# Kernel tuning notes

Hardware: AMD Instinct MI355X
Metric: run time of the kernel (lower is better)

## Reference

```python
import jax, jax.numpy as jnp
import numpy as np

H = 128          # controller hidden size
NCELL = 8        # memory cells
CS = 8           # cell size
R = 1            # read heads
L = 16           # stacked DNC layers
E = 15           # embedding size
NCLS = 30
NUMFRI = 5
NN_IN = H + R * CS                   # 136, controller input width (layers > 0)
XI = R * CS + 3 * CS + 5 * R + 3     # 40, interface vector size
CLIP = 20.0
EPS = 1e-6
B, T = 128, 64
NOT_EYE = 1.0 - np.eye(NCELL, dtype=np.float32)


def setup_inputs() -> dict:
    key = jax.random.key(0)
    ks = iter(jax.random.split(key, 40))
    n = lambda shape, s=0.05: jax.random.normal(next(ks), shape, dtype=jnp.float32) * s
    return {
        "x": jax.random.randint(next(ks), (B, T), 0, NCLS, dtype=jnp.int32),
        "f": n((B, H * NUMFRI), 1.0),
        "embed": n((NCLS + 3, E), 1.0),
        # LSTM controller: [layer, sublayer(2), 4H, in] with in padded to NN_IN
        "W_ih": n((L, 2, 4 * H, NN_IN)),
        "W_hh": n((L, 2, 4 * H, H)),
        "b_ih": n((L, 2, 4 * H)),
        "b_hh": n((L, 2, 4 * H)),
        "W_if": n((XI, H)),            # memory interface
        "b_if": n((XI,)),
        "W_out": n((H, NN_IN)),        # final DNC output linear
        "b_out": n((H,)),
        "W_fri": n((H, H * NUMFRI)),
        "b_fri": n((H,)),
        "W_c1": n((H, 2 * H)),
        "b_c1": n((H,)),
        "W_c2": n((NCLS, H)),
        "b_c2": n((NCLS,)),
    }


def lstm_cell(x, h, c, wih, whh, bih, bhh):
    g = x @ wih.T + h @ whh.T + bih + bhh
    i, f, gg, o = jnp.split(g, 4, axis=-1)  # torch gate order i,f,g,o
    c2 = jax.nn.sigmoid(f) * c + jax.nn.sigmoid(i) * jnp.tanh(gg)
    h2 = jax.nn.sigmoid(o) * jnp.tanh(c2)
    return h2, c2


def content_weight(mem, keys, strengths):
    # cosine similarity between keys [b,h,cs] and memory rows [b,m,cs]
    mn = mem / (jnp.linalg.norm(mem, axis=2, keepdims=True) + EPS)
    kn = keys / (jnp.linalg.norm(keys, axis=2, keepdims=True) + EPS)
    sim = jnp.einsum('bhc,bmc->bhm', kn, mn)
    return jax.nn.softmax(sim * strengths[:, :, None], axis=2)


def allocate(usage):
    u = EPS + (1.0 - EPS) * usage
    phi = jnp.argsort(u, axis=1)          # free list (ascending usage)
    su = jnp.take_along_axis(u, phi, axis=1)
    shifted = jnp.cumprod(jnp.concatenate([jnp.ones_like(su[:, :1]), su], axis=1), axis=1)[:, :-1]
    sa = (1.0 - su) * shifted
    phi_rev = jnp.argsort(phi, axis=1)    # inverse permutation
    return jnp.take_along_axis(sa, phi_rev, axis=1)[:, None, :]   # [b,1,m]


def memory_step(xi, mstate):
    mem, link, prec, rw, ww, usage = mstate
    b = xi.shape[0]
    rk = jnp.tanh(xi[:, :R * CS].reshape(b, R, CS))
    rs = jax.nn.softplus(xi[:, R * CS:R * CS + R])
    wk = jnp.tanh(xi[:, R * CS + R:R * CS + R + CS].reshape(b, 1, CS))
    ws = jax.nn.softplus(xi[:, R * CS + R + CS:R * CS + R + CS + 1])
    er = jax.nn.sigmoid(xi[:, R * CS + R + CS + 1:R * CS + R + 2 * CS + 1].reshape(b, 1, CS))
    wv = jnp.tanh(xi[:, R * CS + R + 2 * CS + 1:R * CS + R + 3 * CS + 1].reshape(b, 1, CS))
    fg = jax.nn.sigmoid(xi[:, R * CS + R + 3 * CS + 1:R * CS + 2 * R + 3 * CS + 1])
    ag = jax.nn.sigmoid(xi[:, R * CS + 2 * R + 3 * CS + 1:R * CS + 2 * R + 3 * CS + 2])
    wg = jax.nn.sigmoid(xi[:, R * CS + 2 * R + 3 * CS + 2:R * CS + 2 * R + 3 * CS + 3])
    modes = jax.nn.softmax(xi[:, R * CS + 2 * R + 3 * CS + 3:].reshape(b, R, 3), axis=-1)
    # --- write ---
    usage = usage + (1 - usage) * (1 - jnp.prod(1 - ww, axis=1))
    psi = jnp.prod(1 - fg[:, :, None] * rw, axis=1)
    usage = usage * psi
    wcw = content_weight(mem, wk, ws)                  # [b,1,m]
    alloc = allocate(usage)
    a3 = ag[:, :, None]; g3 = wg[:, :, None]
    ww = g3 * (a3 * alloc + (1 - a3) * wcw)            # [b,1,m]
    reset = jnp.prod(1 - ww[:, :, :, None] * er[:, :, None, :], axis=1)  # [b,m,cs]
    mem = mem * reset + jnp.einsum('bhm,bhc->bmc', ww, wv)
    ww_i = ww[:, :, :, None]; ww_j = ww[:, :, None, :]
    link = (1 - ww_i - ww_j) * link + ww_i * prec[:, :, None, :]
    link = link * NOT_EYE[None, None]
    prec = (1 - jnp.sum(ww, axis=2, keepdims=True)) * prec + ww
    # --- read ---
    cw = content_weight(mem, rk, rs)                   # [b,r,m]
    fwdw = jnp.einsum('bhij,brj->brhi', link, rw)      # forward weightings
    bwdw = jnp.einsum('bri,bhij->brhj', rw, link)      # backward weightings
    rw = (modes[:, :, 2:3] * cw
          + jnp.sum(modes[:, :, 1:2][:, :, :, None] * fwdw, axis=2)
          + jnp.sum(modes[:, :, 0:1][:, :, :, None] * bwdw, axis=2))
    read_vecs = jnp.einsum('brm,bmc->brc', rw, mem).reshape(b, R * CS)
    return read_vecs, (mem, link, prec, rw, ww, usage)


def _forward(x, f, embed, W_ih, W_hh, b_ih, b_hh, W_if, b_if, W_out, b_out,
             W_fri, b_fri, W_c1, b_c1, W_c2, b_c2):
    b = x.shape[0]
    emb = embed[x]                                     # [b,t,E]
    carry0 = (jnp.zeros((L, 2, b, H), jnp.float32), jnp.zeros((L, 2, b, H), jnp.float32),
              jnp.zeros((b, NCELL, CS), jnp.float32), jnp.zeros((b, 1, NCELL, NCELL), jnp.float32),
              jnp.zeros((b, 1, NCELL), jnp.float32), jnp.zeros((b, R, NCELL), jnp.float32),
              jnp.zeros((b, 1, NCELL), jnp.float32), jnp.zeros((b, NCELL), jnp.float32))

    def step(carry, x_t):
        h, c, mem, link, prec, rw, ww, usage = carry
        inp = x_t   # layer-0 sees [x_t, zero initial read] (reset_experience=True); zeros come from padding
        hs, cs = [], []
        for l in range(L):
            xin = jnp.pad(inp, ((0, 0), (0, NN_IN - inp.shape[1])))
            h0, c0 = lstm_cell(xin, h[l, 0], c[l, 0], W_ih[l, 0], W_hh[l, 0], b_ih[l, 0], b_hh[l, 0])
            xin1 = jnp.pad(h0, ((0, 0), (0, NN_IN - H)))
            h1, c1 = lstm_cell(xin1, h[l, 1], c[l, 1], W_ih[l, 1], W_hh[l, 1], b_ih[l, 1], b_hh[l, 1])
            hs.append(jnp.stack([h0, h1])); cs.append(jnp.stack([c0, c1]))
            out = jnp.clip(h1, -CLIP, CLIP)
            xi = out @ W_if.T + b_if
            read_vecs, (mem, link, prec, rw, ww, usage) = memory_step(xi, (mem, link, prec, rw, ww, usage))
            inp = jnp.concatenate([out, read_vecs], axis=1)   # [b, 136] -> next layer
        y = inp @ W_out.T + b_out
        return (jnp.stack(hs), jnp.stack(cs), mem, link, prec, rw, ww, usage), y

    _, ys = jax.lax.scan(step, carry0, emb.transpose(1, 0, 2))
    z = ys[-1]                                         # encoder output = last timestep [b,H]
    f_out = jax.nn.relu(f @ W_fri.T + b_fri)
    hcat = jnp.concatenate([z, f_out], axis=1)         # [b,2H]
    h1 = jax.nn.relu(hcat @ W_c1.T + b_c1)
    return h1 @ W_c2.T + b_c2                          # [b, n_class]


def reference(x, f, embed, W_ih, W_hh, b_ih, b_hh, W_if, b_if, W_out, b_out,
              W_fri, b_fri, W_c1, b_c1, W_c2, b_c2):
    return _forward(x, f, embed, W_ih, W_hh, b_ih, b_hh, W_if, b_if, W_out, b_out,
                    W_fri, b_fri, W_c1, b_c1, W_c2, b_c2)
```

## Files before the change

kernel.cpp:

```cpp
#include <hip/hip_runtime.h>
#include <stdint.h>

#define LNUM 16
#define H 128
#define TT 64
#define NCLSN 30
#define EPSF 1e-6f

typedef _Float16 half2v __attribute__((ext_vector_type(2)));

__device__ inline float fdot2(uint32_t a, uint32_t b, float c) {
  return __builtin_amdgcn_fdot2(__builtin_bit_cast(half2v, a),
                                __builtin_bit_cast(half2v, b), c, false);
}
__device__ inline float dot8(uint4 w, uint4 xv, float a) {
  a = fdot2(w.x, xv.x, a); a = fdot2(w.y, xv.y, a);
  a = fdot2(w.z, xv.z, a); a = fdot2(w.w, xv.w, a);
  return a;
}
__device__ __forceinline__ float rcpf(float x) { return __builtin_amdgcn_rcpf(x); }
__device__ inline float sigf(float x) { return rcpf(1.0f + __expf(-x)); }
__device__ __forceinline__ float tanh_fast(float x) {
  float xc = fminf(fmaxf(x, -15.f), 15.f);
  float e = __expf(2.f * xc);
  return (e - 1.f) * rcpf(e + 1.f);
}
__device__ __forceinline__ float softplus_fast(float x) {
  return fmaxf(x, 0.f) + __logf(1.f + __expf(-fabsf(x)));
}
__device__ inline uint32_t packh2(float a, float b) {
  half2v h; h.x = (_Float16)a; h.y = (_Float16)b;
  return __builtin_bit_cast(uint32_t, h);
}
__device__ inline uint16_t f16bits(float a) {
  _Float16 h = (_Float16)a;
  return __builtin_bit_cast(uint16_t, h);
}
__device__ __forceinline__ void gl_lds16(const uint4* g, uint4* l) {
  __builtin_amdgcn_global_load_lds(
      (const __attribute__((address_space(1))) void*)g,
      (__attribute__((address_space(3))) void*)l, 16, 0, 0);
}
__device__ __forceinline__ void bar_lgkm() {
  asm volatile("s_waitcnt lgkmcnt(0)\ns_barrier" ::: "memory");
}

__global__ void prepA(const float* __restrict__ W_ih, const float* __restrict__ W_hh,
                      uint4* __restrict__ WB) {
  int idx = blockIdx.x * 256 + threadIdx.x;
  int lc = idx / 16896;
  int r  = idx % 16896;
  int row, kq;
  if (r < 16384) {
    int q = r >> 11;
    int rem = r & 2047;
    int g = rem >> 9;
    int gt = rem & 511;
    int j = gt >> 2, s = gt & 3;
    kq = s + 4 * q;
    row = g * 128 + j;
  } else {
    int r2 = r - 16384;
    int g = r2 >> 7, j = r2 & 127;
    kq = 32; row = g * 128 + j;
  }
  bool zero = ((lc & 1) && kq == 16);
  uint32_t p[4];
#pragma unroll
  for (int i2 = 0; i2 < 4; i2++) {
    float w0 = 0.f, w1 = 0.f;
    if (!zero) {
      int k0 = 8 * kq + 2 * i2;
      w0 = (k0 < 136) ? W_ih[((size_t)lc * 512 + row) * 136 + k0]
                      : W_hh[((size_t)lc * 512 + row) * 128 + (k0 - 136)];
      w1 = (k0 + 1 < 136) ? W_ih[((size_t)lc * 512 + row) * 136 + k0 + 1]
                          : W_hh[((size_t)lc * 512 + row) * 128 + (k0 + 1 - 136)];
    }
    p[i2] = packh2(w0, w1);
  }
  uint4 v; v.x = p[0]; v.y = p[1]; v.z = p[2]; v.w = p[3];
  WB[idx] = v;
}

__global__ void prepB(const float* __restrict__ b_ih, const float* __restrict__ b_hh,
                      const float* __restrict__ W_if, const float* __restrict__ W_fri,
                      const float* __restrict__ W_c1, const float* __restrict__ W_c2,
                      float* __restrict__ bias_comb, uint32_t* __restrict__ Wif16,
                      float* __restrict__ WfriT, float* __restrict__ Wc1T,
                      float* __restrict__ Wc2T) {
  int idx = blockIdx.x * 256 + threadIdx.x;
  if (idx < 16384) { bias_comb[idx] = b_ih[idx] + b_hh[idx]; return; }
  idx -= 16384;
  if (idx < 2560)  {
    int j = idx / 64, k2 = idx % 64;
    Wif16[idx] = packh2(W_if[j * 128 + 2 * k2], W_if[j * 128 + 2 * k2 + 1]);
    return;
  }
  idx -= 2560;
  if (idx < 81920) { int k = idx / 128, j = idx % 128; WfriT[idx] = W_fri[j * 640 + k]; return; }
  idx -= 81920;
  if (idx < 32768) { int k = idx / 128, j = idx % 128; Wc1T[idx]  = W_c1[j * 256 + k]; return; }
  idx -= 32768;
  if (idx < 3840)  { int k = idx / 30,  j = idx % 30;  Wc2T[idx]  = W_c2[j * 128 + k]; return; }
}

__device__ __forceinline__ void memstep_par(
    int m, const float* __restrict__ xi,
    float (&mm)[8], float (&lkr)[8],
    float& u, float& p, float& r, float& w,
    float (&rv)[8]) {
  float rk[8], wk[8], er[8], wv[8];
#pragma unroll
  for (int c = 0; c < 8; c++) {
    rk[c] = tanh_fast(xi[c]);
    wk[c] = tanh_fast(xi[9 + c]);
    er[c] = sigf(xi[18 + c]);
    wv[c] = tanh_fast(xi[26 + c]);
  }
  float rs  = softplus_fast(xi[8]);
  float wsd = softplus_fast(xi[17]);
  float fg  = sigf(xi[34]), ag = sigf(xi[35]), wg = sigf(xi[36]);
  float l0 = xi[37], l1 = xi[38], l2 = xi[39];
  float lmx = fmaxf(l0, fmaxf(l1, l2));
  float eb = __expf(l0 - lmx), ef = __expf(l1 - lmx), ec = __expf(l2 - lmx);
  float minv = rcpf(eb + ef + ec);
  float mode_b = eb * minv, mode_f = ef * minv, mode_c = ec * minv;

  u = u + (1.f - u) * w;
  u *= (1.f - fg * r);

  float kn2 = 0.f, mn2 = 0.f, dp = 0.f;
#pragma unroll
  for (int c = 0; c < 8; c++) { kn2 += wk[c]*wk[c]; mn2 += mm[c]*mm[c]; dp += wk[c]*mm[c]; }
  float sim = dp * rcpf((sqrtf(kn2) + EPSF) * (sqrtf(mn2) + EPSF)) * wsd;
  float mx = sim;
  mx = fmaxf(mx, __shfl_xor(mx, 1));
  mx = fmaxf(mx, __shfl_xor(mx, 2));
  mx = fmaxf(mx, __shfl_xor(mx, 4));
  float e = __expf(sim - mx);
  float se = e;
  se += __shfl_xor(se, 1); se += __shfl_xor(se, 2); se += __shfl_xor(se, 4);
  float wcw = e * rcpf(se);

  float up = EPSF + (1.f - EPSF) * u;
  float prod = 1.f;
#pragma unroll
  for (int n = 0; n < 8; n++) {
    float un = __shfl(up, n);
    bool before = (un < up) || (un == up && n < m);
    prod *= ((n != m) && before) ? un : 1.f;
  }
  float alloc = (1.f - up) * prod;
  float wn = wg * (ag * alloc + (1.f - ag) * wcw);
  float sw = wn;
  sw += __shfl_xor(sw, 1); sw += __shfl_xor(sw, 2); sw += __shfl_xor(sw, 4);

#pragma unroll
  for (int c = 0; c < 8; c++)
    mm[c] = mm[c] * (1.f - wn * er[c]) + wn * wv[c];

  float wnv[8], pvv[8];
#pragma unroll
  for (int n = 0; n < 8; n++) { wnv[n] = __shfl(wn, n); pvv[n] = __shfl(p, n); }
#pragma unroll
  for (int jj = 0; jj < 8; jj++)
    lkr[jj] = (jj == m) ? 0.f : ((1.f - wn - wnv[jj]) * lkr[jj] + wn * pvv[jj]);
  p = (1.f - sw) * p + wn;

  float rn2 = 0.f; mn2 = 0.f; dp = 0.f;
#pragma unroll
  for (int c = 0; c < 8; c++) { rn2 += rk[c]*rk[c]; mn2 += mm[c]*mm[c]; dp += rk[c]*mm[c]; }
  float sim2 = dp * rcpf((sqrtf(rn2) + EPSF) * (sqrtf(mn2) + EPSF)) * rs;
  float mx2 = sim2;
  mx2 = fmaxf(mx2, __shfl_xor(mx2, 1));
  mx2 = fmaxf(mx2, __shfl_xor(mx2, 2));
  mx2 = fmaxf(mx2, __shfl_xor(mx2, 4));
  float e2 = __expf(sim2 - mx2);
  float se2 = e2;
  se2 += __shfl_xor(se2, 1); se2 += __shfl_xor(se2, 2); se2 += __shfl_xor(se2, 4);
  float cw = e2 * rcpf(se2);

  float rv8[8];
#pragma unroll
  for (int n = 0; n < 8; n++) rv8[n] = __shfl(r, n);
  float fwd = 0.f;
#pragma unroll
  for (int jj = 0; jj < 8; jj++) fwd += lkr[jj] * rv8[jj];
  float bw[8];
#pragma unroll
  for (int jj = 0; jj < 8; jj++) bw[jj] = r * lkr[jj];
#pragma unroll
  for (int jj = 0; jj < 8; jj++) {
    bw[jj] += __shfl_xor(bw[jj], 1);
    bw[jj] += __shfl_xor(bw[jj], 2);
    bw[jj] += __shfl_xor(bw[jj], 4);
  }
  bool s1 = (m & 1) != 0, s2 = (m & 2) != 0, s4 = (m & 4) != 0;
  float t0 = s1 ? bw[1] : bw[0];
  float t1 = s1 ? bw[3] : bw[2];
  float t2 = s1 ? bw[5] : bw[4];
  float t3 = s1 ? bw[7] : bw[6];
  float q0 = s2 ? t1 : t0;
  float q1 = s2 ? t3 : t2;
  float bwd = s4 ? q1 : q0;

  float rn = mode_c * cw + mode_f * fwd + mode_b * bwd;

#pragma unroll
  for (int c = 0; c < 8; c++) rv[c] = rn * mm[c];
#pragma unroll
  for (int c = 0; c < 8; c++) {
    rv[c] += __shfl_xor(rv[c], 1);
    rv[c] += __shfl_xor(rv[c], 2);
    rv[c] += __shfl_xor(rv[c], 4);
  }
  r = rn; w = wn;
}

__device__ __forceinline__ void aux_work(
    int lane, bool write_inp,
    const uint4 (&wreg)[16], const float* __restrict__ b_if,
    const uint4* __restrict__ outhu4, float* __restrict__ xi_lds,
    uint4* __restrict__ inpu4,
    float (&mm)[8], float (&lkr)[8],
    float& u, float& p, float& r, float& w,
    float (&rv)[8]) {
  if (lane < 40) {
    float acc0 = 0.f;
#pragma unroll
    for (int q = 0; q < 16; q++) acc0 = dot8(wreg[q], outhu4[q], acc0);
    xi_lds[lane] = acc0 + b_if[lane];
  }
  asm volatile("s_waitcnt lgkmcnt(0)" ::: "memory");
  __builtin_amdgcn_sched_barrier(0);
  __builtin_amdgcn_wave_barrier();
  if (lane < 8) {
    memstep_par(lane, xi_lds, mm, lkr, u, p, r, w, rv);
    if (write_inp && lane == 0) {
      uint4 pv4;
      pv4.x = packh2(rv[0], rv[1]); pv4.y = packh2(rv[2], rv[3]);
      pv4.z = packh2(rv[4], rv[5]); pv4.w = packh2(rv[6], rv[7]);
      inpu4[16] = pv4;
    }
  }
}

#define STAGE(lcX, qX, bbX)                                                    \
  do {                                                                         \
    const uint4* sp_ = WB + (size_t)(lcX) * 16896 + (size_t)(qX) * 2048 + tid; \
    uint4* dp_ = myslab + (size_t)(bbX) * 256;                                 \
    gl_lds16(sp_,        dp_);                                                 \
    gl_lds16(sp_ + 512,  dp_ + 64);                                            \
    gl_lds16(sp_ + 1024, dp_ + 128);                                           \
    gl_lds16(sp_ + 1536, dp_ + 192);                                           \
  } while (0)

__global__ __launch_bounds__(576) void dnc_main(
    const int* __restrict__ x, const float* __restrict__ embed,
    const uint4* __restrict__ WB, const float* __restrict__ bias_comb,
    const uint32_t* __restrict__ Wif16, const float* __restrict__ b_if,
    const float* __restrict__ W_out, const float* __restrict__ b_out,
    float* __restrict__ y_buf) {
  __shared__ __align__(16) uint16_t hst[32 * 128];
  __shared__ float c_st[32 * 128];
  __shared__ float emb_lds[495];
  __shared__ __align__(16) uint32_t inp16[17 * 4];
  __shared__ __align__(16) uint16_t outh16[128];
  __shared__ float inp_f32[128];
  __shared__ float xi_lds[40];
  __shared__ float rv_f32[8];
  __shared__ __align__(16) uint4 sbuf[8 * 4 * 256];

  uint4* inpu4 = (uint4*)inp16;
  uint4* hstu4 = (uint4*)hst;
  uint4* outhu4 = (uint4*)outh16;
  uint16_t* inpu16 = (uint16_t*)inp16;

  const int tid = threadIdx.x;
  const int b0 = blockIdx.x;
  const int ln = tid & 63;
  uint4* myslab = sbuf + (size_t)(tid >> 6) * 1024;

  float mm[8] = {0.f,0.f,0.f,0.f,0.f,0.f,0.f,0.f};
  float lkr[8] = {0.f,0.f,0.f,0.f,0.f,0.f,0.f,0.f};
  float p_u = 0.f, p_p = 0.f, p_r = 0.f, p_w = 0.f;
  float rvout[8];

  uint4 wreg[16];
  if (tid >= 512 && (tid & 63) < 40) {
    const uint4* wr = (const uint4*)(Wif16 + (tid & 63) * 64);
#pragma unroll
    for (int q = 0; q < 16; q++) wreg[q] = wr[q];
  }

  for (int i = tid; i < 32 * 128; i += 576) { hst[i] = 0; c_st[i] = 0.f; }
  for (int i = tid; i < 495; i += 576) emb_lds[i] = embed[i];
  __syncthreads();
  if (tid < 17) {
    int q = tid;
    int ix = x[b0 * TT + 0];
    uint32_t p0, p1, p2, p3;
    {
      int k0 = 8 * q;
      float e0 = (k0 < 15) ? emb_lds[ix * 15 + k0] : 0.f;
      float e1 = (k0 + 1 < 15) ? emb_lds[ix * 15 + k0 + 1] : 0.f;
      float e2 = (k0 + 2 < 15) ? emb_lds[ix * 15 + k0 + 2] : 0.f;
      float e3 = (k0 + 3 < 15) ? emb_lds[ix * 15 + k0 + 3] : 0.f;
      float e4 = (k0 + 4 < 15) ? emb_lds[ix * 15 + k0 + 4] : 0.f;
      float e5 = (k0 + 5 < 15) ? emb_lds[ix * 15 + k0 + 5] : 0.f;
      float e6 = (k0 + 6 < 15) ? emb_lds[ix * 15 + k0 + 6] : 0.f;
      float e7 = (k0 + 7 < 15) ? emb_lds[ix * 15 + k0 + 7] : 0.f;
      p0 = packh2(e0, e1); p1 = packh2(e2, e3); p2 = packh2(e4, e5); p3 = packh2(e6, e7);
    }
    uint4 v; v.x = p0; v.y = p1; v.z = p2; v.w = p3;
    inpu4[q] = v;
  }
  if (tid < 512) { STAGE(0, 0, 0); STAGE(0, 1, 1); STAGE(0, 2, 2); }
  __syncthreads();

  for (int t = 0; t < TT; ++t) {
    for (int l = 0; l < LNUM; ++l) {
      const int lc0 = l * 2, lc1 = l * 2 + 1;
      const int nlc0 = (l == 15) ? 0 : lc0 + 2;
      const int j = tid >> 2, s = tid & 3;
      float aA0 = 0.f, aA1 = 0.f, aA2 = 0.f, aA3 = 0.f;
      uint4 wd0 = {}, wd1 = {}, wd2 = {}, wd3 = {};
      float bA0 = 0.f, bA1 = 0.f, bA2 = 0.f, bA3 = 0.f;

      if (tid < 512) {
        uint4 wt0 = {}, wt1 = {}, wt2 = {}, wt3 = {};
        if (s == 0) {
          const uint4* wt = WB + (size_t)lc0 * 16896 + 16384 + j;
          wt0 = wt[0]; wt1 = wt[128]; wt2 = wt[256]; wt3 = wt[384];
        }
        if (s == 0) {
          const float* bb = bias_comb + lc0 * 512 + j;
          bA0 = bb[0]; bA1 = bb[128]; bA2 = bb[256]; bA3 = bb[384];
        }
#pragma unroll
        for (int q = 0; q < 8; q++) {
          if (q < 5) STAGE(lc0, q + 3, (q + 3) & 3);
          else       STAGE(lc1, q - 5, (q + 3) & 3);
          asm volatile("s_waitcnt vmcnt(12)" ::: "memory");
          __builtin_amdgcn_sched_barrier(0);
          const uint4* wb = myslab + (size_t)(q & 3) * 256 + ln;
          uint4 w0 = wb[0], w1 = wb[64], w2 = wb[128], w3 = wb[192];
          int kq = s + 4 * q;
          bool defer = (s == 0) && (q == 4);
          int kqe = defer ? 0 : kq;
          const uint4* xp = (kqe < 17) ? (inpu4 + kqe)
                                       : (hstu4 + lc0 * 16 + (kqe - 17));
          uint4 xv0 = *xp;
          if (defer) { wd0 = w0; wd1 = w1; wd2 = w2; wd3 = w3; }
          else {
            aA0 = dot8(w0, xv0, aA0);
            aA1 = dot8(w1, xv0, aA1);
            aA2 = dot8(w2, xv0, aA2);
            aA3 = dot8(w3, xv0, aA3);
          }
        }
        if (s == 0) {
          uint4 xv0 = hstu4[lc0 * 16 + 15];
          aA0 = dot8(wt0, xv0, aA0);
          aA1 = dot8(wt1, xv0, aA1);
          aA2 = dot8(wt2, xv0, aA2);
          aA3 = dot8(wt3, xv0, aA3);
        }
      } else if (t > 0 || l > 0) {
        const int lane = tid - 512;
        aux_work(lane, (l != 0), wreg, b_if, outhu4, xi_lds,
                 inpu4, mm, lkr, p_u, p_p, p_r, p_w, rvout);
      }
      bar_lgkm();

      if (tid < 512) {
        if (s == 0) {
          uint4 xr0 = inpu4[16];
          aA0 = dot8(wd0, xr0, aA0);
          aA1 = dot8(wd1, xr0, aA1);
          aA2 = dot8(wd2, xr0, aA2);
          aA3 = dot8(wd3, xr0, aA3);
        }
        aA0 += __shfl_xor(aA0, 1); aA0 += __shfl_xor(aA0, 2);
        aA1 += __shfl_xor(aA1, 1); aA1 += __shfl_xor(aA1, 2);
        aA2 += __shfl_xor(aA2, 1); aA2 += __shfl_xor(aA2, 2);
        aA3 += __shfl_xor(aA3, 1); aA3 += __shfl_xor(aA3, 2);
        if (s == 0) {
          float gi = aA0 + bA0, gf = aA1 + bA1, gg = aA2 + bA2, go = aA3 + bA3;
          int ci = lc0 * 128 + j;
          float c2 = sigf(gf) * c_st[ci] + sigf(gi) * tanh_fast(gg);
          c_st[ci] = c2;
          hst[ci] = f16bits(sigf(go) * tanh_fast(c2));
        }
      }
      bar_lgkm();

      if (tid < 512) {
        float cA0 = 0.f, cA1 = 0.f, cA2 = 0.f, cA3 = 0.f;
        uint4 wt0 = {}, wt1 = {}, wt2 = {}, wt3 = {};
        float bC0 = 0.f, bC1 = 0.f, bC2 = 0.f, bC3 = 0.f;
        if (s == 0) {
          const uint4* wt = WB + (size_t)lc1 * 16896 + 16384 + j;
          wt0 = wt[0]; wt1 = wt[128]; wt2 = wt[256]; wt3 = wt[384];
          const float* bb = bias_comb + lc1 * 512 + j;
          bC0 = bb[0]; bC1 = bb[128]; bC2 = bb[256]; bC3 = bb[384];
        }
#pragma unroll
        for (int q = 0; q < 8; q++) {
          if (q < 5) STAGE(lc1, q + 3, (q + 3) & 3);
          else       STAGE(nlc0, q - 5, (q + 3) & 3);
          asm volatile("s_waitcnt vmcnt(12)" ::: "memory");
          __builtin_amdgcn_sched_barrier(0);
          const uint4* wb = myslab + (size_t)(q & 3) * 256 + ln;
          uint4 w0 = wb[0], w1 = wb[64], w2 = wb[128], w3 = wb[192];
          int kq = s + 4 * q;
          const uint4* xp = (kq < 17) ? (hstu4 + lc0 * 16 + kq)
                                      : (hstu4 + lc1 * 16 + (kq - 17));
          uint4 xv0 = *xp;
          cA0 = dot8(w0, xv0, cA0);
          cA1 = dot8(w1, xv0, cA1);
          cA2 = dot8(w2, xv0, cA2);
          cA3 = dot8(w3, xv0, cA3);
        }
        if (s == 0) {
          uint4 xv0 = hstu4[lc1 * 16 + 15];
          cA0 = dot8(wt0, xv0, cA0);
          cA1 = dot8(wt1, xv0, cA1);
          cA2 = dot8(wt2, xv0, cA2);
          cA3 = dot8(wt3, xv0, cA3);
        }
        cA0 += __shfl_xor(cA0, 1); cA0 += __shfl_xor(cA0, 2);
        cA1 += __shfl_xor(cA1, 1); cA1 += __shfl_xor(cA1, 2);
        cA2 += __shfl_xor(cA2, 1); cA2 += __shfl_xor(cA2, 2);
        cA3 += __shfl_xor(cA3, 1); cA3 += __shfl_xor(cA3, 2);
        if (s == 0) {
          float gi = cA0 + bC0, gf = cA1 + bC1, gg = cA2 + bC2, go = cA3 + bC3;
          int ci = lc1 * 128 + j;
          float c2 = sigf(gf) * c_st[ci] + sigf(gi) * tanh_fast(gg);
          c_st[ci] = c2;
          float h2 = sigf(go) * tanh_fast(c2);
          hst[ci] = f16bits(h2);
          inp_f32[j] = h2;
          outh16[j] = f16bits(h2);
          if (l != 15) inpu16[j] = f16bits(h2);
        }
        if (l == 15 && t < 63 && tid >= 448 && tid < 465) {
          int q = tid - 448;
          int ix = x[b0 * TT + t + 1];
          uint32_t p0, p1, p2, p3;
          {
            int k0 = 8 * q;
            float e0 = (k0 < 15) ? emb_lds[ix * 15 + k0] : 0.f;
            float e1 = (k0 + 1 < 15) ? emb_lds[ix * 15 + k0 + 1] : 0.f;
            float e2 = (k0 + 2 < 15) ? emb_lds[ix * 15 + k0 + 2] : 0.f;
            float e3 = (k0 + 3 < 15) ? emb_lds[ix * 15 + k0 + 3] : 0.f;
            float e4 = (k0 + 4 < 15) ? emb_lds[ix * 15 + k0 + 4] : 0.f;
            float e5 = (k0 + 5 < 15) ? emb_lds[ix * 15 + k0 + 5] : 0.f;
            float e6 = (k0 + 6 < 15) ? emb_lds[ix * 15 + k0 + 6] : 0.f;
            float e7 = (k0 + 7 < 15) ? emb_lds[ix * 15 + k0 + 7] : 0.f;
            p0 = packh2(e0, e1); p1 = packh2(e2, e3); p2 = packh2(e4, e5); p3 = packh2(e6, e7);
          }
          uint4 v; v.x = p0; v.y = p1; v.z = p2; v.w = p3;
          inpu4[q] = v;
        }
      }
      bar_lgkm();
    }
  }

  if (tid >= 512) {
    const int lane = tid - 512;
    aux_work(lane, false, wreg, b_if, outhu4, xi_lds,
             inpu4, mm, lkr, p_u, p_p, p_r, p_w, rvout);
    if (lane == 0) {
#pragma unroll
      for (int c = 0; c < 8; c++) rv_f32[c] = rvout[c];
    }
  }
  __syncthreads();
  if (tid < 128) {
    int i = tid;
    float a = b_out[i];
    for (int k = 0; k < 128; ++k) a += inp_f32[k] * W_out[i * 136 + k];
    for (int k = 0; k < 8; ++k)   a += rv_f32[k] * W_out[i * 136 + 128 + k];
    y_buf[b0 * H + i] = a;
  }
}

__global__ void head_kernel(const float* __restrict__ y_buf, const float* __restrict__ f,
                            const float* __restrict__ WfriT, const float* __restrict__ b_fri,
                            const float* __restrict__ Wc1T, const float* __restrict__ b_c1,
                            const float* __restrict__ Wc2T, const float* __restrict__ b_c2,
                            float* __restrict__ out) {
  __shared__ float fl[640], yl[128], fo[128], h1l[128];
  int b = blockIdx.x, j = threadIdx.x;
  for (int i = j; i < 640; i += 128) fl[i] = f[b * 640 + i];
  yl[j] = y_buf[b * 128 + j];
  __syncthreads();
  float a = b_fri[j];
  for (int k = 0; k < 640; ++k) a += fl[k] * WfriT[k * 128 + j];
  fo[j] = fmaxf(a, 0.f);
  __syncthreads();
  float a2 = b_c1[j];
  for (int k = 0; k < 128; ++k) a2 += yl[k] * Wc1T[k * 128 + j];
  for (int k = 0; k < 128; ++k) a2 += fo[k] * Wc1T[(128 + k) * 128 + j];
  h1l[j] = fmaxf(a2, 0.f);
  __syncthreads();
  if (j < NCLSN) {
    float a3 = b_c2[j];
    for (int k = 0; k < 128; ++k) a3 += h1l[k] * Wc2T[k * NCLSN + j];
    out[b * NCLSN + j] = a3;
  }
}

extern "C" void kernel_launch(void* const* d_in, const int* in_sizes, int n_in,
                              void* d_out, int out_size, void* d_ws, size_t ws_size,
                              hipStream_t stream) {
  const int*   x     = (const int*)d_in[0];
  const float* f     = (const float*)d_in[1];
  const float* embed = (const float*)d_in[2];
  const float* W_ih  = (const float*)d_in[3];
  const float* W_hh  = (const float*)d_in[4];
  const float* b_ih  = (const float*)d_in[5];
  const float* b_hh  = (const float*)d_in[6];
  const float* W_if  = (const float*)d_in[7];
  const float* b_if  = (const float*)d_in[8];
  const float* W_out = (const float*)d_in[9];
  const float* b_out = (const float*)d_in[10];
  const float* W_fri = (const float*)d_in[11];
  const float* b_fri = (const float*)d_in[12];
  const float* W_c1  = (const float*)d_in[13];
  const float* b_c1  = (const float*)d_in[14];
  const float* W_c2  = (const float*)d_in[15];
  const float* b_c2  = (const float*)d_in[16];

  uint8_t* ws = (uint8_t*)d_ws;
  uint4* WB        = (uint4*)(ws + 0);
  float* bias_comb = (float*)(ws + 8650752);
  uint32_t* Wif16  = (uint32_t*)(ws + 8716288);
  float* WfriT     = (float*)(ws + 8726528);
  float* Wc1T      = (float*)(ws + 9054208);
  float* Wc2T      = (float*)(ws + 9185280);
  float* y_buf     = (float*)(ws + 9200640);
  float* out       = (float*)d_out;

  prepA<<<2112, 256, 0, stream>>>(W_ih, W_hh, WB);
  prepB<<<537, 256, 0, stream>>>(b_ih, b_hh, W_if, W_fri, W_c1, W_c2,
                                 bias_comb, Wif16, WfriT, Wc1T, Wc2T);
  dnc_main<<<128, 576, 0, stream>>>(x, embed, WB, bias_comb, Wif16, b_if,
                                    W_out, b_out, y_buf);
  head_kernel<<<128, 128, 0, stream>>>(y_buf, f, WfriT, b_fri, Wc1T, b_c1,
                                       Wc2T, b_c2, out);
}
```

Measured before the change: 10.06 ms.

## Stream LSTM weights directly into registers instead of staging through LDS

Replaces the global_load_lds staging of LSTM weight slabs with inline-asm global_load_dwordx4 into a 4-deep register ring, keeping the same vmcnt(12) prefetch distance. Biases, interface weights and b_if are moved into LDS once at kernel start, replacing per-step global bias loads and the aux wave's register-held weights. The embedding write for the next timestep moves to the aux wave. This drops the LDS round-trip for weights but raises register pressure in a 576-thread block, and relies on asm volatile ordering for the vmcnt waits to stay correct.

```diff
diff --git a/kernel.cpp b/kernel.cpp
--- a/kernel.cpp
+++ b/kernel.cpp
@@ -36,11 +36,15 @@
   _Float16 h = (_Float16)a;
   return __builtin_bit_cast(uint16_t, h);
 }
-__device__ __forceinline__ void gl_lds16(const uint4* g, uint4* l) {
-  __builtin_amdgcn_global_load_lds(
-      (const __attribute__((address_space(1))) void*)g,
-      (__attribute__((address_space(3))) void*)l, 16, 0, 0);
-}
+__device__ __forceinline__ uint4 gload4(const uint4* sbase, uint32_t voff_bytes) {
+  uint4 r;
+  asm volatile("global_load_dwordx4 %0, %1, %2"
+               : "=v"(r) : "v"(voff_bytes), "s"(sbase) : "memory");
+  return r;
+}
+#define WAIT12() do { \
+  asm volatile("s_waitcnt vmcnt(12)" ::: "memory"); \
+  __builtin_amdgcn_sched_barrier(0); } while (0)
 __device__ __forceinline__ void bar_lgkm() {
   asm volatile("s_waitcnt lgkmcnt(0)\ns_barrier" ::: "memory");
 }
@@ -219,7 +223,7 @@
 
 __device__ __forceinline__ void aux_work(
     int lane, bool write_inp,
-    const uint4 (&wreg)[16], const float* __restrict__ b_if,
+    const uint4* __restrict__ wifu4, const float* __restrict__ bif_lds,
     const uint4* __restrict__ outhu4, float* __restrict__ xi_lds,
     uint4* __restrict__ inpu4,
     float (&mm)[8], float (&lkr)[8],
@@ -227,9 +231,10 @@
     float (&rv)[8]) {
   if (lane < 40) {
     float acc0 = 0.f;
-#pragma unroll
-    for (int q = 0; q < 16; q++) acc0 = dot8(wreg[q], outhu4[q], acc0);
-    xi_lds[lane] = acc0 + b_if[lane];
+    const uint4* wr = wifu4 + lane * 16;
+#pragma unroll
+    for (int q = 0; q < 16; q++) acc0 = dot8(wr[q], outhu4[q], acc0);
+    xi_lds[lane] = acc0 + bif_lds[lane];
   }
   asm volatile("s_waitcnt lgkmcnt(0)" ::: "memory");
   __builtin_amdgcn_sched_barrier(0);
@@ -245,16 +250,6 @@
   }
 }
 
-#define STAGE(lcX, qX, bbX)                                                    \
-  do {                                                                         \
-    const uint4* sp_ = WB + (size_t)(lcX) * 16896 + (size_t)(qX) * 2048 + tid; \
-    uint4* dp_ = myslab + (size_t)(bbX) * 256;                                 \
-    gl_lds16(sp_,        dp_);                                                 \
-    gl_lds16(sp_ + 512,  dp_ + 64);                                            \
-    gl_lds16(sp_ + 1024, dp_ + 128);                                           \
-    gl_lds16(sp_ + 1536, dp_ + 192);                                           \
-  } while (0)
-
 __global__ __launch_bounds__(576) void dnc_main(
     const int* __restrict__ x, const float* __restrict__ embed,
     const uint4* __restrict__ WB, const float* __restrict__ bias_comb,
@@ -263,38 +258,36 @@
     float* __restrict__ y_buf) {
   __shared__ __align__(16) uint16_t hst[32 * 128];
   __shared__ float c_st[32 * 128];
+  __shared__ float bias_lds[32 * 512];
+  __shared__ __align__(16) uint32_t wif_lds[2560];
+  __shared__ float bif_lds[40];
   __shared__ float emb_lds[495];
   __shared__ __align__(16) uint32_t inp16[17 * 4];
   __shared__ __align__(16) uint16_t outh16[128];
   __shared__ float inp_f32[128];
   __shared__ float xi_lds[40];
   __shared__ float rv_f32[8];
-  __shared__ __align__(16) uint4 sbuf[8 * 4 * 256];
 
   uint4* inpu4 = (uint4*)inp16;
   uint4* hstu4 = (uint4*)hst;
   uint4* outhu4 = (uint4*)outh16;
   uint16_t* inpu16 = (uint16_t*)inp16;
+  const uint4* wifu4 = (const uint4*)wif_lds;
 
   const int tid = threadIdx.x;
   const int b0 = blockIdx.x;
-  const int ln = tid & 63;
-  uint4* myslab = sbuf + (size_t)(tid >> 6) * 1024;
+  const uint32_t vo16 = (uint32_t)tid * 16u;
 
   float mm[8] = {0.f,0.f,0.f,0.f,0.f,0.f,0.f,0.f};
   float lkr[8] = {0.f,0.f,0.f,0.f,0.f,0.f,0.f,0.f};
   float p_u = 0.f, p_p = 0.f, p_r = 0.f, p_w = 0.f;
   float rvout[8];
 
-  uint4 wreg[16];
-  if (tid >= 512 && (tid & 63) < 40) {
-    const uint4* wr = (const uint4*)(Wif16 + (tid & 63) * 64);
-#pragma unroll
-    for (int q = 0; q < 16; q++) wreg[q] = wr[q];
-  }
-
   for (int i = tid; i < 32 * 128; i += 576) { hst[i] = 0; c_st[i] = 0.f; }
+  for (int i = tid; i < 16384; i += 576) bias_lds[i] = bias_comb[i];
+  for (int i = tid; i < 2560; i += 576) wif_lds[i] = Wif16[i];
   for (int i = tid; i < 495; i += 576) emb_lds[i] = embed[i];
+  if (tid < 40) bif_lds[tid] = b_if[tid];
   __syncthreads();
   if (tid < 17) {
     int q = tid;
@@ -315,36 +308,49 @@
     uint4 v; v.x = p0; v.y = p1; v.z = p2; v.w = p3;
     inpu4[q] = v;
   }
-  if (tid < 512) { STAGE(0, 0, 0); STAGE(0, 1, 1); STAGE(0, 2, 2); }
   __syncthreads();
+
+  uint4 wbuf[4][4];
+  if (tid < 512) {
+#pragma unroll
+    for (int p5 = 0; p5 < 3; p5++) {
+#pragma unroll
+      for (int g = 0; g < 4; g++)
+        wbuf[p5][g] = gload4(WB, (uint32_t)((p5 * 2048 + g * 512) * 16) + vo16);
+    }
+  }
 
   for (int t = 0; t < TT; ++t) {
     for (int l = 0; l < LNUM; ++l) {
       const int lc0 = l * 2, lc1 = l * 2 + 1;
       const int nlc0 = (l == 15) ? 0 : lc0 + 2;
       const int j = tid >> 2, s = tid & 3;
+      const uint4* baseA = WB + (size_t)lc0 * 16896;
+      const uint4* baseC = WB + (size_t)lc1 * 16896;
+      const uint4* baseN = WB + (size_t)nlc0 * 16896;
       float aA0 = 0.f, aA1 = 0.f, aA2 = 0.f, aA3 = 0.f;
-      uint4 wd0 = {}, wd1 = {}, wd2 = {}, wd3 = {};
-      float bA0 = 0.f, bA1 = 0.f, bA2 = 0.f, bA3 = 0.f;
+      uint4 wd0, wd1, wd2, wd3;
+      uint4 wt0, wt1, wt2, wt3;
 
       if (tid < 512) {
-        uint4 wt0 = {}, wt1 = {}, wt2 = {}, wt3 = {};
-        if (s == 0) {
-          const uint4* wt = WB + (size_t)lc0 * 16896 + 16384 + j;
-          wt0 = wt[0]; wt1 = wt[128]; wt2 = wt[256]; wt3 = wt[384];
-        }
-        if (s == 0) {
-          const float* bb = bias_comb + lc0 * 512 + j;
-          bA0 = bb[0]; bA1 = bb[128]; bA2 = bb[256]; bA3 = bb[384];
+        if (s == 0) {
+          uint32_t tb = (uint32_t)((16384 + j) * 16);
+          wt0 = gload4(baseA, tb);
+          wt1 = gload4(baseA, tb + 128 * 16);
+          wt2 = gload4(baseA, tb + 256 * 16);
+          wt3 = gload4(baseA, tb + 384 * 16);
         }
 #pragma unroll
         for (int q = 0; q < 8; q++) {
-          if (q < 5) STAGE(lc0, q + 3, (q + 3) & 3);
-          else       STAGE(lc1, q - 5, (q + 3) & 3);
-          asm volatile("s_waitcnt vmcnt(12)" ::: "memory");
-          __builtin_amdgcn_sched_barrier(0);
-          const uint4* wb = myslab + (size_t)(q & 3) * 256 + ln;
-          uint4 w0 = wb[0], w1 = wb[64], w2 = wb[128], w3 = wb[192];
+          const int pp = q + 3;
+          const uint4* sb = (pp < 8) ? baseA : baseC;
+          const int ppl = (pp < 8) ? pp : pp - 8;
+#pragma unroll
+          for (int g = 0; g < 4; g++)
+            wbuf[pp & 3][g] = gload4(sb, (uint32_t)((ppl * 2048 + g * 512) * 16) + vo16);
+          WAIT12();
+          uint4 w0 = wbuf[q & 3][0], w1 = wbuf[q & 3][1];
+          uint4 w2 = wbuf[q & 3][2], w3 = wbuf[q & 3][3];
           int kq = s + 4 * q;
           bool defer = (s == 0) && (q == 4);
           int kqe = defer ? 0 : kq;
@@ -367,9 +373,8 @@
           aA3 = dot8(wt3, xv0, aA3);
         }
       } else if (t > 0 || l > 0) {
-        const int lane = tid - 512;
-        aux_work(lane, (l != 0), wreg, b_if, outhu4, xi_lds,
-                 inpu4, mm, lkr, p_u, p_p, p_r, p_w, rvout);
+        aux_work(tid - 512, (l != 0), wifu4, bif_lds, outhu4,
+                 xi_lds, inpu4, mm, lkr, p_u, p_p, p_r, p_w, rvout);
       }
       bar_lgkm();
 
@@ -386,7 +391,8 @@
         aA2 += __shfl_xor(aA2, 1); aA2 += __shfl_xor(aA2, 2);
         aA3 += __shfl_xor(aA3, 1); aA3 += __shfl_xor(aA3, 2);
         if (s == 0) {
-          float gi = aA0 + bA0, gf = aA1 + bA1, gg = aA2 + bA2, go = aA3 + bA3;
+          const float* bb = bias_lds + lc0 * 512 + j;
+          float gi = aA0 + bb[0], gf = aA1 + bb[128], gg = aA2 + bb[256], go = aA3 + bb[384];
           int ci = lc0 * 128 + j;
           float c2 = sigf(gf) * c_st[ci] + sigf(gi) * tanh_fast(gg);
           c_st[ci] = c2;
@@ -397,22 +403,24 @@
 
       if (tid < 512) {
         float cA0 = 0.f, cA1 = 0.f, cA2 = 0.f, cA3 = 0.f;
-        uint4 wt0 = {}, wt1 = {}, wt2 = {}, wt3 = {};
-        float bC0 = 0.f, bC1 = 0.f, bC2 = 0.f, bC3 = 0.f;
-        if (s == 0) {
-          const uint4* wt = WB + (size_t)lc1 * 16896 + 16384 + j;
-          wt0 = wt[0]; wt1 = wt[128]; wt2 = wt[256]; wt3 = wt[384];
-          const float* bb = bias_comb + lc1 * 512 + j;
-          bC0 = bb[0]; bC1 = bb[128]; bC2 = bb[256]; bC3 = bb[384];
+        if (s == 0) {
+          uint32_t tb = (uint32_t)((16384 + j) * 16);
+          wt0 = gload4(baseC, tb);
+          wt1 = gload4(baseC, tb + 128 * 16);
+          wt2 = gload4(baseC, tb + 256 * 16);
+          wt3 = gload4(baseC, tb + 384 * 16);
         }
 #pragma unroll
         for (int q = 0; q < 8; q++) {
-          if (q < 5) STAGE(lc1, q + 3, (q + 3) & 3);
-          else       STAGE(nlc0, q - 5, (q + 3) & 3);
-          asm volatile("s_waitcnt vmcnt(12)" ::: "memory");
-          __builtin_amdgcn_sched_barrier(0);
-          const uint4* wb = myslab + (size_t)(q & 3) * 256 + ln;
-          uint4 w0 = wb[0], w1 = wb[64], w2 = wb[128], w3 = wb[192];
+          const int pp = q + 3;
+          const uint4* sb = (pp < 8) ? baseC : baseN;
+          const int ppl = (pp < 8) ? pp : pp - 8;
+#pragma unroll
+          for (int g = 0; g < 4; g++)
+            wbuf[pp & 3][g] = gload4(sb, (uint32_t)((ppl * 2048 + g * 512) * 16) + vo16);
+          WAIT12();
+          uint4 w0 = wbuf[q & 3][0], w1 = wbuf[q & 3][1];
+          uint4 w2 = wbuf[q & 3][2], w3 = wbuf[q & 3][3];
           int kq = s + 4 * q;
           const uint4* xp = (kq < 17) ? (hstu4 + lc0 * 16 + kq)
                                       : (hstu4 + lc1 * 16 + (kq - 17));
@@ -434,7 +442,8 @@
         cA2 += __shfl_xor(cA2, 1); cA2 += __shfl_xor(cA2, 2);
         cA3 += __shfl_xor(cA3, 1); cA3 += __shfl_xor(cA3, 2);
         if (s == 0) {
-          float gi = cA0 + bC0, gf = cA1 + bC1, gg = cA2 + bC2, go = cA3 + bC3;
+          const float* bb = bias_lds + lc1 * 512 + j;
+          float gi = cA0 + bb[0], gf = cA1 + bb[128], gg = cA2 + bb[256], go = cA3 + bb[384];
           int ci = lc1 * 128 + j;
           float c2 = sigf(gf) * c_st[ci] + sigf(gi) * tanh_fast(gg);
           c_st[ci] = c2;
@@ -444,8 +453,10 @@
           outh16[j] = f16bits(h2);
           if (l != 15) inpu16[j] = f16bits(h2);
         }
-        if (l == 15 && t < 63 && tid >= 448 && tid < 465) {
-          int q = tid - 448;
+      } else {
+        const int lane = tid - 512;
+        if (l == 15 && t < 63 && lane < 17) {
+          int q = lane;
           int ix = x[b0 * TT + t + 1];
           uint32_t p0, p1, p2, p3;
           {
@@ -469,10 +480,9 @@
   }
 
   if (tid >= 512) {
-    const int lane = tid - 512;
-    aux_work(lane, false, wreg, b_if, outhu4, xi_lds,
-             inpu4, mm, lkr, p_u, p_p, p_r, p_w, rvout);
-    if (lane == 0) {
+    aux_work(tid - 512, false, wifu4, bif_lds, outhu4,
+             xi_lds, inpu4, mm, lkr, p_u, p_p, p_r, p_w, rvout);
+    if (tid == 512) {
 #pragma unroll
       for (int c = 0; c < 8; c++) rv_f32[c] = rvout[c];
     }
```

Result: slower. 19.32 ms (+92.1%).
